# Optimization experiments

Measured on AMD Instinct MI355X. Metric: run time of the kernel, lower is better.

Reference implementation:

```python
import jax, jax.numpy as jnp
import numpy as np

NUM_HEADS = 8
LN_EPS = 1e-5


def setup_inputs() -> dict:
    key = jax.random.key(0)
    ks = jax.random.split(key, 8)
    B, H, W, C = 2, 64, 64, 256
    return {
        "x": jax.random.normal(ks[0], (B, H, W, C), dtype=jnp.float32),
        "cond": jax.random.normal(ks[1], (B, C), dtype=jnp.float32),
        "t": jax.random.randint(ks[2], (B,), 0, 100, dtype=jnp.int64),
        "emb_table": jax.random.normal(ks[3], (100, C), dtype=jnp.float32) * 0.02,
        "ada_w": jax.random.normal(ks[4], (C, 2 * C), dtype=jnp.float32) * 0.02,
        "ada_b": jnp.zeros((2 * C,), dtype=jnp.float32),
        "qkv_w": jax.random.normal(ks[5], (C, 3 * C), dtype=jnp.float32) * 0.02,
        "qkv_b": jnp.zeros((3 * C,), dtype=jnp.float32),
        "proj_w": jax.random.normal(ks[6], (C, C), dtype=jnp.float32) * 0.02,
        "proj_b": jnp.zeros((C,), dtype=jnp.float32),
    }


def reference(x, cond, t, emb_table, ada_w, ada_b, qkv_w, qkv_b, proj_w, proj_b):
    B, H, W, C = x.shape
    N = H * W
    h = NUM_HEADS
    d = C // h
    scale = d ** -0.5

    x = x.reshape(B, N, C)

    # AdaLayerNorm (adalayernorm_abs): timestep embedding -> SiLU -> Linear -> scale/shift
    emb = emb_table[t]                                # [B, C]
    ss = jax.nn.silu(emb) @ ada_w + ada_b             # [B, 2C]
    sc, sh = jnp.split(ss, 2, axis=-1)                # each [B, C]
    mu = jnp.mean(x, axis=-1, keepdims=True)
    var = jnp.var(x, axis=-1, keepdims=True)
    xn = (x - mu) * jax.lax.rsqrt(var + LN_EPS)       # LN without affine
    x = xn * (1.0 + sc[:, None, :]) + sh[:, None, :]

    # QKV projection and head split
    qkv = (x @ qkv_w + qkv_b).reshape(B, N, 3, h, d)
    qkv = jnp.transpose(qkv, (2, 0, 3, 1, 4))          # [3, B, h, N, d]
    q, k, v = qkv[0], qkv[1], qkv[2]

    # Manual attention: full [B, h, N, N] scores (matches original module)
    attn = jnp.einsum('bhnd,bhmd->bhnm', q, k) * scale
    attn = jax.nn.softmax(attn, axis=-1)
    out = jnp.einsum('bhnm,bhmd->bhnd', attn, v)       # [B, h, N, d]
    out = jnp.transpose(out, (0, 2, 1, 3)).reshape(B, N, C)

    out = (out.reshape(B, H, W, C) @ proj_w) + proj_b
    return out
```

## Files before the change

kernel.cpp:

```cpp
#include <hip/hip_runtime.h>
#include <hip/hip_bf16.h>
#include <stdint.h>

typedef __attribute__((ext_vector_type(8))) short bfrag;
typedef __attribute__((ext_vector_type(4))) short bfrag4;
typedef __attribute__((ext_vector_type(4))) float f32x4;
typedef __attribute__((ext_vector_type(2))) float f32x2;
typedef __attribute__((ext_vector_type(2))) unsigned int u32x2;

__device__ inline short f2bf(float f) {
  union { float f; uint32_t u; } v; v.f = f;
  uint32_t u = v.u;
  uint32_t r = (u + 0x7fffu + ((u >> 16) & 1u)) >> 16;
  return (short)r;
}
__device__ inline float bf2f(short s) {
  return __builtin_bit_cast(float, (uint32_t)((uint32_t)(uint16_t)s << 16));
}

#if __has_builtin(__builtin_amdgcn_cvt_pk_bf16_f32)
typedef __attribute__((ext_vector_type(2))) __bf16 bf16x2_t;
__device__ inline uint32_t pack_bf16(float a, float b) {
  bf16x2_t r = __builtin_amdgcn_cvt_pk_bf16_f32(a, b);
  return __builtin_bit_cast(uint32_t, r);
}
#else
__device__ inline uint32_t pack_bf16(float a, float b) {
  uint32_t ua = __builtin_bit_cast(uint32_t, a) + 0x8000u;
  uint32_t ub = __builtin_bit_cast(uint32_t, b) + 0x8000u;
  return __builtin_amdgcn_perm(ub, ua, 0x07060302);
}
#endif

__global__ __launch_bounds__(256) void prep_kernel(
    const float* __restrict__ emb_table, const int* __restrict__ t,
    const float* __restrict__ ada_w, const float* __restrict__ ada_b,
    float* __restrict__ scsh,
    const float* __restrict__ qkv_w, short* __restrict__ qkv_wt,
    const float* __restrict__ proj_w, short* __restrict__ proj_wt) {
  __shared__ float smem[64 * 65];
  const int blk = blockIdx.x;
  const int tid = threadIdx.x;
  if (blk < 16) {
    float* se = smem;
    float* part = smem + 256;
    int b = blk >> 3, ox = blk & 7;
    int tt = t[b];
    float e = emb_table[tt * 256 + tid];
    se[tid] = e / (1.f + __expf(-e));
    __syncthreads();
    int ol = tid & 63, kc = tid >> 6;
    int o = ox * 64 + ol;
    float acc = 0.f;
#pragma unroll 8
    for (int k = kc * 64; k < (kc + 1) * 64; ++k) acc += se[k] * ada_w[k * 512 + o];
    part[tid] = acc;
    __syncthreads();
    if (tid < 64) {
      int oo = ox * 64 + tid;
      scsh[b * 512 + oo] =
          part[tid] + part[64 + tid] + part[128 + tid] + part[192 + tid] + ada_b[oo];
    }
  } else {
    const float* W; short* Wt; int N, lb;
    if (blk < 64) { W = qkv_w; Wt = qkv_wt; N = 768; lb = blk - 16; }
    else          { W = proj_w; Wt = proj_wt; N = 256; lb = blk - 64; }
    float (*tile)[65] = (float(*)[65])smem;
    int k0 = (lb & 3) * 64, n0 = (lb >> 2) * 64;
    int r = tid >> 2, c0 = (tid & 3) * 16;
    const float* src = W + (long)(k0 + r) * N + n0 + c0;
#pragma unroll
    for (int j = 0; j < 16; j += 4) {
      float4 v = *(const float4*)(src + j);
      tile[r][c0 + j] = v.x; tile[r][c0 + j + 1] = v.y;
      tile[r][c0 + j + 2] = v.z; tile[r][c0 + j + 3] = v.w;
    }
    __syncthreads();
    int nl = tid >> 2, kc = (tid & 3) * 16;
    short outv[16];
#pragma unroll
    for (int j = 0; j < 16; ++j) outv[j] = f2bf(tile[kc + j][nl]);
    short* dst = Wt + (long)(n0 + nl) * 256 + k0 + kc;
    *(bfrag*)dst = *(bfrag*)&outv[0];
    *(bfrag*)(dst + 8) = *(bfrag*)&outv[8];
  }
}

__global__ __launch_bounds__(256) void ln_kernel(const float* __restrict__ x,
                                                 const float* __restrict__ scsh,
                                                 short* __restrict__ xb) {
  int row = blockIdx.x;
  int b = row >> 12;
  int i = threadIdx.x;
  float v = x[(long)row * 256 + i];
  float s = v, sq = v * v;
#pragma unroll
  for (int off = 32; off > 0; off >>= 1) {
    s += __shfl_down(s, off);
    sq += __shfl_down(sq, off);
  }
  __shared__ float red[8];
  int w = i >> 6;
  if ((i & 63) == 0) { red[w] = s; red[4 + w] = sq; }
  __syncthreads();
  s = red[0] + red[1] + red[2] + red[3];
  sq = red[4] + red[5] + red[6] + red[7];
  float mu = s * (1.f / 256.f);
  float var = sq * (1.f / 256.f) - mu * mu;
  float xn = (v - mu) * rsqrtf(var + 1e-5f);
  float y = xn * (1.f + scsh[b * 512 + i]) + scsh[b * 512 + 256 + i];
  xb[(long)row * 256 + i] = f2bf(y);
}

__global__ __launch_bounds__(256) void gemm_bf16(const short* __restrict__ A,
                                                 const short* __restrict__ Bt,
                                                 const float* __restrict__ bias,
                                                 int N, int mode, float qscale,
                                                 short* __restrict__ qk,
                                                 short* __restrict__ vT,
                                                 float* __restrict__ cout) {
  __shared__ short As[128 * 40];
  __shared__ short Bs[64 * 40];
  const int mt = blockIdx.x, nt = blockIdx.y;
  const int tid = threadIdx.x;
  const int w = tid >> 6, lane = tid & 63, l16 = lane & 15, quad = lane >> 4;
  const int ar = tid >> 1, ak = (tid & 1) * 16;
  const int br = tid >> 2, bk = (tid & 3) * 8;
  f32x4 acc[2][4] = {};
  const short* Arow = A + (long)(mt * 128 + ar) * 256 + ak;
  const short* Brow = Bt + (long)(nt * 64 + br) * 256 + bk;
  for (int kk = 0; kk < 8; ++kk) {
    __syncthreads();
    *(bfrag*)&As[ar * 40 + ak] = *(const bfrag*)(Arow + kk * 32);
    *(bfrag*)&As[ar * 40 + ak + 8] = *(const bfrag*)(Arow + kk * 32 + 8);
    *(bfrag*)&Bs[br * 40 + bk] = *(const bfrag*)(Brow + kk * 32);
    __syncthreads();
    bfrag a0 = *(const bfrag*)&As[(w * 32 + l16) * 40 + quad * 8];
    bfrag a1 = *(const bfrag*)&As[(w * 32 + 16 + l16) * 40 + quad * 8];
#pragma unroll
    for (int c = 0; c < 4; ++c) {
      bfrag bf = *(const bfrag*)&Bs[(c * 16 + l16) * 40 + quad * 8];
      acc[0][c] = __builtin_amdgcn_mfma_f32_16x16x32_bf16(a0, bf, acc[0][c], 0, 0, 0);
      acc[1][c] = __builtin_amdgcn_mfma_f32_16x16x32_bf16(a1, bf, acc[1][c], 0, 0, 0);
    }
  }
  const int rowb = mt * 128 + w * 32 + quad * 4;
  if (mode == 1) {
#pragma unroll
    for (int rg = 0; rg < 2; ++rg) {
      int row0 = rowb + rg * 16;
#pragma unroll
      for (int c = 0; c < 4; ++c) {
        int col = nt * 64 + c * 16 + l16;
        float bv = bias[col];
#pragma unroll
        for (int r = 0; r < 4; ++r)
          cout[(long)(row0 + r) * N + col] = acc[rg][c][r] + bv;
      }
    }
  } else if (nt < 8) {
#pragma unroll
    for (int rg = 0; rg < 2; ++rg) {
      int row0 = rowb + rg * 16;
#pragma unroll
      for (int c = 0; c < 4; ++c) {
        int col = nt * 64 + c * 16 + l16;
        float bv = bias[col];
        float mult = (col < 256) ? qscale : 1.0f;
#pragma unroll
        for (int r = 0; r < 4; ++r)
          qk[(long)(row0 + r) * 512 + col] = f2bf((acc[rg][c][r] + bv) * mult);
      }
    }
  } else {
    const int bb = mt >> 5;
#pragma unroll
    for (int rg = 0; rg < 2; ++rg) {
      int keyl = (rowb + rg * 16) & 4095;
#pragma unroll
      for (int c = 0; c < 4; ++c) {
        int col = nt * 64 + c * 16 + l16;
        float bv = bias[col];
        int d = col - 512;
        u32x2 dd;
        dd.x = pack_bf16(acc[rg][c][0] + bv, acc[rg][c][1] + bv);
        dd.y = pack_bf16(acc[rg][c][2] + bv, acc[rg][c][3] + bv);
        *(u32x2*)&vT[((long)(bb * 8 + (d >> 5)) * 32 + (d & 31)) * 4096 + keyl] = dd;
      }
    }
  }
}

__global__ __launch_bounds__(256) void attn_kernel(const short* __restrict__ qk,
                                                   const short* __restrict__ vT,
                                                   short* __restrict__ OpB,
                                                   float* __restrict__ lpart) {
  const int blk = blockIdx.x;
  const int qt = blk & 31;
  const int bh = (blk >> 5) & 15;
  const int ks = blk >> 9;
  const int b = bh >> 3, hh = bh & 7;
  const int tid = threadIdx.x;
  const int w = tid >> 6, lane = tid & 63, l16 = lane & 15, quad = lane >> 4;

  __shared__ short Ks[2][64 * 40];
  __shared__ short Vt[2][32 * 68];

  const long rowbase = (long)b * 4096;
  const int qrow0 = qt * 128 + w * 32 + l16;
  bfrag qf0 = *(const bfrag*)&qk[(rowbase + qrow0) * 512 + hh * 32 + quad * 8];
  bfrag qf1 = *(const bfrag*)&qk[(rowbase + qrow0 + 16) * 512 + hh * 32 + quad * 8];

  f32x4 o00 = {0,0,0,0}, o10 = {0,0,0,0};
  f32x4 o01 = {0,0,0,0}, o11 = {0,0,0,0};
  f32x2 l0 = {0.f, 0.f}, l1 = {0.f, 0.f};

  const int si = tid >> 2, sk = (tid & 3) * 8;
  const int vrow = tid >> 3, vcol = (tid & 7) * 8;
  const short* ksrc = qk + rowbase * 512 + 256 + hh * 32 + (long)si * 512 + sk;
  const short* vsrc = vT + ((long)bh * 32 + vrow) * 4096 + vcol;

  const int kt0 = ks * 16;
  bfrag k8 = *(const bfrag*)(ksrc + (long)kt0 * 64 * 512);
  bfrag v8 = *(const bfrag*)(vsrc + kt0 * 64);

  int buf = 0;
  for (int i = 0; i < 16; ++i) {
    *(bfrag*)&Ks[buf][si * 40 + sk] = k8;
    *(bfrag*)&Vt[buf][vrow * 68 + vcol] = v8;
    int nn = (i < 15) ? (i + 1) : 15;
    k8 = *(const bfrag*)(ksrc + (long)(kt0 + nn) * 64 * 512);
    v8 = *(const bfrag*)(vsrc + (kt0 + nn) * 64);
    __syncthreads();

    f32x4 s0[4], s1[4];
#pragma unroll
    for (int nt = 0; nt < 4; ++nt) {
      bfrag kf = *(const bfrag*)&Ks[buf][(nt * 16 + l16) * 40 + quad * 8];
      f32x4 z = {0,0,0,0};
      s0[nt] = __builtin_amdgcn_mfma_f32_16x16x32_bf16(kf, qf0, z, 0, 0, 0);
      s1[nt] = __builtin_amdgcn_mfma_f32_16x16x32_bf16(kf, qf1, z, 0, 0, 0);
    }
    bfrag4 pb0[4], pb1[4];
#pragma unroll
    for (int nt = 0; nt < 4; ++nt) {
      float a0 = __builtin_amdgcn_exp2f(s0[nt][0]);
      float a1 = __builtin_amdgcn_exp2f(s0[nt][1]);
      float a2 = __builtin_amdgcn_exp2f(s0[nt][2]);
      float a3 = __builtin_amdgcn_exp2f(s0[nt][3]);
      f32x2 pa = {a0, a1}, pc = {a2, a3};
      l0 += pa; l0 += pc;
      u32x2 pk0; pk0.x = pack_bf16(a0, a1); pk0.y = pack_bf16(a2, a3);
      pb0[nt] = __builtin_bit_cast(bfrag4, pk0);
      float b0 = __builtin_amdgcn_exp2f(s1[nt][0]);
      float b1 = __builtin_amdgcn_exp2f(s1[nt][1]);
      float b2 = __builtin_amdgcn_exp2f(s1[nt][2]);
      float b3 = __builtin_amdgcn_exp2f(s1[nt][3]);
      f32x2 pb = {b0, b1}, pd = {b2, b3};
      l1 += pb; l1 += pd;
      u32x2 pk1; pk1.x = pack_bf16(b0, b1); pk1.y = pack_bf16(b2, b3);
      pb1[nt] = __builtin_bit_cast(bfrag4, pk1);
    }
#pragma unroll
    for (int nt = 0; nt < 4; ++nt) {
      bfrag4 va = *(const bfrag4*)&Vt[buf][l16 * 68 + nt * 16 + quad * 4];
      bfrag4 vb = *(const bfrag4*)&Vt[buf][(16 + l16) * 68 + nt * 16 + quad * 4];
      o00 = __builtin_amdgcn_mfma_f32_16x16x16bf16_1k(va, pb0[nt], o00, 0, 0, 0);
      o10 = __builtin_amdgcn_mfma_f32_16x16x16bf16_1k(vb, pb0[nt], o10, 0, 0, 0);
      o01 = __builtin_amdgcn_mfma_f32_16x16x16bf16_1k(va, pb1[nt], o01, 0, 0, 0);
      o11 = __builtin_amdgcn_mfma_f32_16x16x16bf16_1k(vb, pb1[nt], o11, 0, 0, 0);
    }
    buf ^= 1;
  }
  float ls0 = l0.x + l0.y, ls1 = l1.x + l1.y;
  ls0 += __shfl_xor(ls0, 16); ls0 += __shfl_xor(ls0, 32);
  ls1 += __shfl_xor(ls1, 16); ls1 += __shfl_xor(ls1, 32);
  const long pb0 = (((long)ks * 16 + bh) * 4096 + qrow0) * 32;
  const long pb1 = pb0 + 16 * 32;
  u32x2 dA, dB, dC, dD;
  dA.x = pack_bf16(o00[0], o00[1]); dA.y = pack_bf16(o00[2], o00[3]);
  dB.x = pack_bf16(o10[0], o10[1]); dB.y = pack_bf16(o10[2], o10[3]);
  dC.x = pack_bf16(o01[0], o01[1]); dC.y = pack_bf16(o01[2], o01[3]);
  dD.x = pack_bf16(o11[0], o11[1]); dD.y = pack_bf16(o11[2], o11[3]);
  *(u32x2*)&OpB[pb0 + quad * 4] = dA;
  *(u32x2*)&OpB[pb0 + 16 + quad * 4] = dB;
  *(u32x2*)&OpB[pb1 + quad * 4] = dC;
  *(u32x2*)&OpB[pb1 + 16 + quad * 4] = dD;
  if (quad == 0) {
    lpart[((long)ks * 16 + bh) * 4096 + qrow0] = ls0;
    lpart[((long)ks * 16 + bh) * 4096 + qrow0 + 16] = ls1;
  }
}

__global__ __launch_bounds__(256) void reduce_kernel(const short* __restrict__ OpB,
                                                     const float* __restrict__ lpart,
                                                     short* __restrict__ attn_out) {
  int row = blockIdx.x;
  int bq = row >> 12, q = row & 4095;
  int d = threadIdx.x;
  int h2 = d >> 5, dd = d & 31;
  int bh = bq * 8 + h2;
  float s = 0.f, l = 0.f;
#pragma unroll
  for (int ks = 0; ks < 4; ++ks) {
    long base = (long)(ks * 16 + bh) * 4096 + q;
    s += bf2f(OpB[base * 32 + dd]);
    l += lpart[base];
  }
  attn_out[(long)row * 256 + d] = f2bf(s / l);
}

extern "C" void kernel_launch(void* const* d_in, const int* in_sizes, int n_in,
                              void* d_out, int out_size, void* d_ws, size_t ws_size,
                              hipStream_t stream) {
  const float* x      = (const float*)d_in[0];
  const int*   t      = (const int*)d_in[2];
  const float* emb    = (const float*)d_in[3];
  const float* ada_w  = (const float*)d_in[4];
  const float* ada_b  = (const float*)d_in[5];
  const float* qkv_w  = (const float*)d_in[6];
  const float* qkv_b  = (const float*)d_in[7];
  const float* proj_w = (const float*)d_in[8];
  const float* proj_b = (const float*)d_in[9];

  char* ws = (char*)d_ws;
  float* scsh     = (float*)(ws);
  short* qkv_wt   = (short*)(ws + 4096);
  short* proj_wt  = (short*)(ws + 397312);
  short* xb       = (short*)(ws + 528384);
  short* qk_out   = (short*)(ws + 4722688);
  short* vT       = (short*)(ws + 13111296);
  short* attn_out = (short*)(ws + 17305600);
  short* OpB      = (short*)(ws + 21499904);
  float* lpart    = (float*)(ws + 38277120);

  const float QS = 0.17677669529663687f * 1.4426950408889634f;

  prep_kernel<<<80, 256, 0, stream>>>(emb, t, ada_w, ada_b, scsh,
                                      qkv_w, qkv_wt, proj_w, proj_wt);
  ln_kernel<<<8192, 256, 0, stream>>>(x, scsh, xb);
  gemm_bf16<<<dim3(64, 12), 256, 0, stream>>>(xb, qkv_wt, qkv_b, 768, 0, QS,
                                              qk_out, vT, nullptr);
  attn_kernel<<<2048, 256, 0, stream>>>(qk_out, vT, OpB, lpart);
  reduce_kernel<<<8192, 256, 0, stream>>>(OpB, lpart, attn_out);
  gemm_bf16<<<dim3(64, 4), 256, 0, stream>>>(attn_out, proj_wt, proj_b, 256, 1,
                                             1.0f, nullptr, nullptr, (float*)d_out);
}
```

Measured before the change: 172.7 us.

## Double query rows per attention block, prefetch GEMM tiles, vectorize layernorm

The attention kernel now handles 256 query rows per block, 64 per wave, using four Q fragments per wave. Each K/V tile loaded into shared memory is therefore reused by twice as many queries, and the grid is halved. The score-to-P-to-O pipeline is also interleaved per key sub-tile. The GEMM register-prefetches the next K slice while the MFMAs run. LayerNorm uses one wave per row with float4 loads and drops the shared-memory reduction and block barrier. The trade-offs are higher register pressure and fewer blocks in the attention kernel, which may lower occupancy.

```diff
diff --git a/kernel.cpp b/kernel.cpp
--- a/kernel.cpp
+++ b/kernel.cpp
@@ -89,27 +89,29 @@
 __global__ __launch_bounds__(256) void ln_kernel(const float* __restrict__ x,
                                                  const float* __restrict__ scsh,
                                                  short* __restrict__ xb) {
-  int row = blockIdx.x;
+  int row = blockIdx.x * 4 + (threadIdx.x >> 6);
   int b = row >> 12;
-  int i = threadIdx.x;
-  float v = x[(long)row * 256 + i];
-  float s = v, sq = v * v;
+  int lane = threadIdx.x & 63;
+  float4 v = *(const float4*)(x + (long)row * 256 + lane * 4);
+  float s = v.x + v.y + v.z + v.w;
+  float sq = v.x * v.x + v.y * v.y + v.z * v.z + v.w * v.w;
 #pragma unroll
   for (int off = 32; off > 0; off >>= 1) {
-    s += __shfl_down(s, off);
-    sq += __shfl_down(sq, off);
-  }
-  __shared__ float red[8];
-  int w = i >> 6;
-  if ((i & 63) == 0) { red[w] = s; red[4 + w] = sq; }
-  __syncthreads();
-  s = red[0] + red[1] + red[2] + red[3];
-  sq = red[4] + red[5] + red[6] + red[7];
+    s += __shfl_xor(s, off);
+    sq += __shfl_xor(sq, off);
+  }
   float mu = s * (1.f / 256.f);
   float var = sq * (1.f / 256.f) - mu * mu;
-  float xn = (v - mu) * rsqrtf(var + 1e-5f);
-  float y = xn * (1.f + scsh[b * 512 + i]) + scsh[b * 512 + 256 + i];
-  xb[(long)row * 256 + i] = f2bf(y);
+  float rstd = rsqrtf(var + 1e-5f);
+  const float* scp = scsh + b * 512 + lane * 4;
+  float4 sc = *(const float4*)scp;
+  float4 sh = *(const float4*)(scp + 256);
+  float y0 = (v.x - mu) * rstd * (1.f + sc.x) + sh.x;
+  float y1 = (v.y - mu) * rstd * (1.f + sc.y) + sh.y;
+  float y2 = (v.z - mu) * rstd * (1.f + sc.z) + sh.z;
+  float y3 = (v.w - mu) * rstd * (1.f + sc.w) + sh.w;
+  u32x2 o; o.x = pack_bf16(y0, y1); o.y = pack_bf16(y2, y3);
+  *(u32x2*)&xb[(long)row * 256 + lane * 4] = o;
 }
 
 __global__ __launch_bounds__(256) void gemm_bf16(const short* __restrict__ A,
@@ -129,12 +131,19 @@
   f32x4 acc[2][4] = {};
   const short* Arow = A + (long)(mt * 128 + ar) * 256 + ak;
   const short* Brow = Bt + (long)(nt * 64 + br) * 256 + bk;
+  bfrag a8a = *(const bfrag*)Arow;
+  bfrag a8b = *(const bfrag*)(Arow + 8);
+  bfrag b8  = *(const bfrag*)Brow;
   for (int kk = 0; kk < 8; ++kk) {
     __syncthreads();
-    *(bfrag*)&As[ar * 40 + ak] = *(const bfrag*)(Arow + kk * 32);
-    *(bfrag*)&As[ar * 40 + ak + 8] = *(const bfrag*)(Arow + kk * 32 + 8);
-    *(bfrag*)&Bs[br * 40 + bk] = *(const bfrag*)(Brow + kk * 32);
-    __syncthreads();
+    *(bfrag*)&As[ar * 40 + ak] = a8a;
+    *(bfrag*)&As[ar * 40 + ak + 8] = a8b;
+    *(bfrag*)&Bs[br * 40 + bk] = b8;
+    __syncthreads();
+    int kn = (kk < 7) ? (kk + 1) : 7;
+    a8a = *(const bfrag*)(Arow + kn * 32);
+    a8b = *(const bfrag*)(Arow + kn * 32 + 8);
+    b8  = *(const bfrag*)(Brow + kn * 32);
     bfrag a0 = *(const bfrag*)&As[(w * 32 + l16) * 40 + quad * 8];
     bfrag a1 = *(const bfrag*)&As[(w * 32 + 16 + l16) * 40 + quad * 8];
 #pragma unroll
@@ -196,9 +205,9 @@
                                                    short* __restrict__ OpB,
                                                    float* __restrict__ lpart) {
   const int blk = blockIdx.x;
-  const int qt = blk & 31;
-  const int bh = (blk >> 5) & 15;
-  const int ks = blk >> 9;
+  const int qt = blk & 15;
+  const int bh = (blk >> 4) & 15;
+  const int ks = blk >> 8;
   const int b = bh >> 3, hh = bh & 7;
   const int tid = threadIdx.x;
   const int w = tid >> 6, lane = tid & 63, l16 = lane & 15, quad = lane >> 4;
@@ -207,13 +216,14 @@
   __shared__ short Vt[2][32 * 68];
 
   const long rowbase = (long)b * 4096;
-  const int qrow0 = qt * 128 + w * 32 + l16;
-  bfrag qf0 = *(const bfrag*)&qk[(rowbase + qrow0) * 512 + hh * 32 + quad * 8];
-  bfrag qf1 = *(const bfrag*)&qk[(rowbase + qrow0 + 16) * 512 + hh * 32 + quad * 8];
-
-  f32x4 o00 = {0,0,0,0}, o10 = {0,0,0,0};
-  f32x4 o01 = {0,0,0,0}, o11 = {0,0,0,0};
-  f32x2 l0 = {0.f, 0.f}, l1 = {0.f, 0.f};
+  const int qrow0 = qt * 256 + w * 64 + l16;
+  bfrag qf[4];
+#pragma unroll
+  for (int g = 0; g < 4; ++g)
+    qf[g] = *(const bfrag*)&qk[(rowbase + qrow0 + g * 16) * 512 + hh * 32 + quad * 8];
+
+  f32x4 o0[4] = {}, o1[4] = {};
+  f32x2 lsum[4] = {};
 
   const int si = tid >> 2, sk = (tid & 3) * 8;
   const int vrow = tid >> 3, vcol = (tid & 7) * 8;
@@ -228,67 +238,54 @@
   for (int i = 0; i < 16; ++i) {
     *(bfrag*)&Ks[buf][si * 40 + sk] = k8;
     *(bfrag*)&Vt[buf][vrow * 68 + vcol] = v8;
+    __syncthreads();
     int nn = (i < 15) ? (i + 1) : 15;
     k8 = *(const bfrag*)(ksrc + (long)(kt0 + nn) * 64 * 512);
     v8 = *(const bfrag*)(vsrc + (kt0 + nn) * 64);
-    __syncthreads();
-
-    f32x4 s0[4], s1[4];
+
 #pragma unroll
     for (int nt = 0; nt < 4; ++nt) {
       bfrag kf = *(const bfrag*)&Ks[buf][(nt * 16 + l16) * 40 + quad * 8];
       f32x4 z = {0,0,0,0};
-      s0[nt] = __builtin_amdgcn_mfma_f32_16x16x32_bf16(kf, qf0, z, 0, 0, 0);
-      s1[nt] = __builtin_amdgcn_mfma_f32_16x16x32_bf16(kf, qf1, z, 0, 0, 0);
-    }
-    bfrag4 pb0[4], pb1[4];
-#pragma unroll
-    for (int nt = 0; nt < 4; ++nt) {
-      float a0 = __builtin_amdgcn_exp2f(s0[nt][0]);
-      float a1 = __builtin_amdgcn_exp2f(s0[nt][1]);
-      float a2 = __builtin_amdgcn_exp2f(s0[nt][2]);
-      float a3 = __builtin_amdgcn_exp2f(s0[nt][3]);
-      f32x2 pa = {a0, a1}, pc = {a2, a3};
-      l0 += pa; l0 += pc;
-      u32x2 pk0; pk0.x = pack_bf16(a0, a1); pk0.y = pack_bf16(a2, a3);
-      pb0[nt] = __builtin_bit_cast(bfrag4, pk0);
-      float b0 = __builtin_amdgcn_exp2f(s1[nt][0]);
-      float b1 = __builtin_amdgcn_exp2f(s1[nt][1]);
-      float b2 = __builtin_amdgcn_exp2f(s1[nt][2]);
-      float b3 = __builtin_amdgcn_exp2f(s1[nt][3]);
-      f32x2 pb = {b0, b1}, pd = {b2, b3};
-      l1 += pb; l1 += pd;
-      u32x2 pk1; pk1.x = pack_bf16(b0, b1); pk1.y = pack_bf16(b2, b3);
-      pb1[nt] = __builtin_bit_cast(bfrag4, pk1);
-    }
-#pragma unroll
-    for (int nt = 0; nt < 4; ++nt) {
+      f32x4 s[4];
+      s[0] = __builtin_amdgcn_mfma_f32_16x16x32_bf16(kf, qf[0], z, 0, 0, 0);
+      s[1] = __builtin_amdgcn_mfma_f32_16x16x32_bf16(kf, qf[1], z, 0, 0, 0);
+      s[2] = __builtin_amdgcn_mfma_f32_16x16x32_bf16(kf, qf[2], z, 0, 0, 0);
+      s[3] = __builtin_amdgcn_mfma_f32_16x16x32_bf16(kf, qf[3], z, 0, 0, 0);
+      bfrag4 pb[4];
+#pragma unroll
+      for (int g = 0; g < 4; ++g) {
+        float p0 = __builtin_amdgcn_exp2f(s[g][0]);
+        float p1 = __builtin_amdgcn_exp2f(s[g][1]);
+        float p2 = __builtin_amdgcn_exp2f(s[g][2]);
+        float p3 = __builtin_amdgcn_exp2f(s[g][3]);
+        f32x2 pa = {p0, p1}, pc = {p2, p3};
+        lsum[g] += pa; lsum[g] += pc;
+        u32x2 pk; pk.x = pack_bf16(p0, p1); pk.y = pack_bf16(p2, p3);
+        pb[g] = __builtin_bit_cast(bfrag4, pk);
+      }
       bfrag4 va = *(const bfrag4*)&Vt[buf][l16 * 68 + nt * 16 + quad * 4];
       bfrag4 vb = *(const bfrag4*)&Vt[buf][(16 + l16) * 68 + nt * 16 + quad * 4];
-      o00 = __builtin_amdgcn_mfma_f32_16x16x16bf16_1k(va, pb0[nt], o00, 0, 0, 0);
-      o10 = __builtin_amdgcn_mfma_f32_16x16x16bf16_1k(vb, pb0[nt], o10, 0, 0, 0);
-      o01 = __builtin_amdgcn_mfma_f32_16x16x16bf16_1k(va, pb1[nt], o01, 0, 0, 0);
-      o11 = __builtin_amdgcn_mfma_f32_16x16x16bf16_1k(vb, pb1[nt], o11, 0, 0, 0);
+#pragma unroll
+      for (int g = 0; g < 4; ++g) {
+        o0[g] = __builtin_amdgcn_mfma_f32_16x16x16bf16_1k(va, pb[g], o0[g], 0, 0, 0);
+        o1[g] = __builtin_amdgcn_mfma_f32_16x16x16bf16_1k(vb, pb[g], o1[g], 0, 0, 0);
+      }
     }
     buf ^= 1;
   }
-  float ls0 = l0.x + l0.y, ls1 = l1.x + l1.y;
-  ls0 += __shfl_xor(ls0, 16); ls0 += __shfl_xor(ls0, 32);
-  ls1 += __shfl_xor(ls1, 16); ls1 += __shfl_xor(ls1, 32);
-  const long pb0 = (((long)ks * 16 + bh) * 4096 + qrow0) * 32;
-  const long pb1 = pb0 + 16 * 32;
-  u32x2 dA, dB, dC, dD;
-  dA.x = pack_bf16(o00[0], o00[1]); dA.y = pack_bf16(o00[2], o00[3]);
-  dB.x = pack_bf16(o10[0], o10[1]); dB.y = pack_bf16(o10[2], o10[3]);
-  dC.x = pack_bf16(o01[0], o01[1]); dC.y = pack_bf16(o01[2], o01[3]);
-  dD.x = pack_bf16(o11[0], o11[1]); dD.y = pack_bf16(o11[2], o11[3]);
-  *(u32x2*)&OpB[pb0 + quad * 4] = dA;
-  *(u32x2*)&OpB[pb0 + 16 + quad * 4] = dB;
-  *(u32x2*)&OpB[pb1 + quad * 4] = dC;
-  *(u32x2*)&OpB[pb1 + 16 + quad * 4] = dD;
-  if (quad == 0) {
-    lpart[((long)ks * 16 + bh) * 4096 + qrow0] = ls0;
-    lpart[((long)ks * 16 + bh) * 4096 + qrow0 + 16] = ls1;
+#pragma unroll
+  for (int g = 0; g < 4; ++g) {
+    float ls = lsum[g].x + lsum[g].y;
+    ls += __shfl_xor(ls, 16); ls += __shfl_xor(ls, 32);
+    const long pbase = (((long)ks * 16 + bh) * 4096 + qrow0 + g * 16) * 32;
+    u32x2 dA, dB;
+    dA.x = pack_bf16(o0[g][0], o0[g][1]); dA.y = pack_bf16(o0[g][2], o0[g][3]);
+    dB.x = pack_bf16(o1[g][0], o1[g][1]); dB.y = pack_bf16(o1[g][2], o1[g][3]);
+    *(u32x2*)&OpB[pbase + quad * 4] = dA;
+    *(u32x2*)&OpB[pbase + 16 + quad * 4] = dB;
+    if (quad == 0)
+      lpart[((long)ks * 16 + bh) * 4096 + qrow0 + g * 16] = ls;
   }
 }
 
@@ -338,10 +335,10 @@
 
   prep_kernel<<<80, 256, 0, stream>>>(emb, t, ada_w, ada_b, scsh,
                                       qkv_w, qkv_wt, proj_w, proj_wt);
-  ln_kernel<<<8192, 256, 0, stream>>>(x, scsh, xb);
+  ln_kernel<<<2048, 256, 0, stream>>>(x, scsh, xb);
   gemm_bf16<<<dim3(64, 12), 256, 0, stream>>>(xb, qkv_wt, qkv_b, 768, 0, QS,
                                               qk_out, vT, nullptr);
-  attn_kernel<<<2048, 256, 0, stream>>>(qk_out, vT, OpB, lpart);
+  attn_kernel<<<1024, 256, 0, stream>>>(qk_out, vT, OpB, lpart);
   reduce_kernel<<<8192, 256, 0, stream>>>(OpB, lpart, attn_out);
   gemm_bf16<<<dim3(64, 4), 256, 0, stream>>>(attn_out, proj_wt, proj_b, 256, 1,
                                              1.0f, nullptr, nullptr, (float*)d_out);
```

Result: no change. 169.7 us (-1.8%).
